# Kernel tuning notes

Measured on AMD Instinct MI355X. Metric: run time of the kernel, lower is better.

## Reference

```python
import jax, jax.numpy as jnp
from jax import lax
import numpy as np

B, N, D = 8, 8192, 64
NPOINT, RADIUS, NSAMPLE = 1024, 0.2, 32
EPS = 1e-5  # BatchNorm eps


def setup_inputs() -> dict:
    key = jax.random.key(0)
    ks = jax.random.split(key, 8)
    inp = {
        "xyz": jax.random.uniform(ks[0], (B, 3, N), dtype=jnp.float32),
        "points": jax.random.normal(ks[1], (B, D, N), dtype=jnp.float32),
    }
    dims = [(3 + D, 64), (64, 64), (64, 128)]
    for i, (ci, co) in enumerate(dims):
        inp[f"w{i}"] = jax.random.normal(ks[2 + i], (co, ci), dtype=jnp.float32) * float(1.0 / np.sqrt(ci))
        inp[f"b{i}"] = jnp.zeros((co,), jnp.float32)
        inp[f"g{i}"] = jnp.ones((co,), jnp.float32)
        inp[f"beta{i}"] = jnp.zeros((co,), jnp.float32)
    return inp


def _fps(xyz):
    # Farthest point sampling. xyz: [B, N, 3] -> idx [B, NPOINT]
    b = xyz.shape[0]

    def step(carry, _):
        dist, farthest = carry  # dist [B,N], farthest [B]
        centroid = jnp.take_along_axis(xyz, farthest[:, None, None], axis=1)  # [B,1,3]
        d = jnp.sum((xyz - centroid) ** 2, axis=-1)  # [B,N]
        dist = jnp.minimum(dist, d)
        return (dist, jnp.argmax(dist, axis=-1).astype(jnp.int32)), farthest

    init = (jnp.full((b, xyz.shape[1]), 1e10, xyz.dtype), jnp.zeros((b,), jnp.int32))
    _, idxs = lax.scan(step, init, None, length=NPOINT)  # [NPOINT, B]
    return idxs.T  # [B, NPOINT]


def _ball_query(new_xyz, xyz):
    # new_xyz: [B,S,3] centers, xyz: [B,N,3] -> neighbor idx [B,S,NSAMPLE]
    n = xyz.shape[1]
    sqr = jnp.sum((new_xyz[:, :, None, :] - xyz[:, None, :, :]) ** 2, axis=-1)  # [B,S,N]
    cand = jnp.where(sqr > RADIUS * RADIUS, n, jnp.arange(n, dtype=jnp.int32))  # N = invalid
    neg_top, _ = lax.top_k(-cand, NSAMPLE)  # smallest NSAMPLE valid indices
    idx = -neg_top  # [B,S,K], ascending; == n where fewer than K neighbors
    first = idx[..., :1]  # pad with first (closest-by-index) valid neighbor
    return jnp.where(idx == n, first, idx)


def reference(xyz, points, w0, b0, g0, beta0, w1, b1, g1, beta1, w2, b2, g2, beta2):
    xyz_t = jnp.transpose(xyz, (0, 2, 1))      # [B,N,3]
    pts_t = jnp.transpose(points, (0, 2, 1))   # [B,N,D]
    fps_idx = _fps(xyz_t)                      # [B,S]
    bidx = jnp.arange(xyz.shape[0])[:, None]
    new_xyz = xyz_t[bidx, fps_idx]             # [B,S,3]
    idx = _ball_query(new_xyz, xyz_t)          # [B,S,K]
    bidx3 = jnp.arange(xyz.shape[0])[:, None, None]
    grouped_xyz = xyz_t[bidx3, idx]            # [B,S,K,3]
    grouped_norm = grouped_xyz - new_xyz[:, :, None, :]
    grouped_pts = pts_t[bidx3, idx]            # [B,S,K,D]
    feat = jnp.concatenate([grouped_norm, grouped_pts], axis=-1)  # [B,S,K,3+D]
    # shared 1x1 Conv + BatchNorm (training-mode batch stats) + ReLU chain
    for w, b, g, bt in ((w0, b0, g0, beta0), (w1, b1, g1, beta1), (w2, b2, g2, beta2)):
        h = jnp.einsum('bskc,oc->bsko', feat, w) + b
        mean = jnp.mean(h, axis=(0, 1, 2), keepdims=True)
        var = jnp.var(h, axis=(0, 1, 2), keepdims=True)
        feat = jax.nn.relu((h - mean) * lax.rsqrt(var + EPS) * g + bt)
    pooled = jnp.max(feat, axis=2)             # max over NSAMPLE -> [B,S,C_out]
    return jnp.transpose(new_xyz, (0, 2, 1)), jnp.transpose(pooled, (0, 2, 1))
```

## Files before the change

kernel.cpp:

```cpp
#include <hip/hip_runtime.h>

#define NB 8
#define NP 8192
#define SP 1024
#define KS 32
#define CD 64
#define MROWS (NB*SP*KS)
#define NCOPY 16

typedef float v2f __attribute__((ext_vector_type(2)));
typedef unsigned long long u64;

template <int CTRL>
__device__ __forceinline__ u64 dpp_max_step(u64 x) {
    int lo = (int)(unsigned)(x & 0xffffffffull);
    int hi = (int)(unsigned)(x >> 32);
    int slo = __builtin_amdgcn_update_dpp(lo, lo, CTRL, 0xf, 0xf, false);
    int shi = __builtin_amdgcn_update_dpp(hi, hi, CTRL, 0xf, 0xf, false);
    u64 y = ((u64)(unsigned)shi << 32) | (unsigned)slo;
    return x > y ? x : y;
}

__global__ __launch_bounds__(512, 1) void k_fps_pre(const float* __restrict__ xyz,
                                                    float* __restrict__ fps_pts,
                                                    float* __restrict__ out_nx,
                                                    const float* __restrict__ points,
                                                    float* __restrict__ pts_t,
                                                    const float* __restrict__ w0,
                                                    const float* __restrict__ w1,
                                                    const float* __restrict__ w2,
                                                    float* __restrict__ Wt0,
                                                    float* __restrict__ Wt1,
                                                    float* __restrict__ Wt2,
                                                    float* __restrict__ stats)
{
#pragma clang fp contract(off)
    __shared__ __align__(16) unsigned char smem[131072 + 256];
    const int blk = blockIdx.x;
    const int t = threadIdx.x;

    if (blk >= NB) {
        if (blk >= NB + NB * (NP / 64)) {
            for (int i = t; i < 8192; i += 512) stats[i] = 0.f;
            for (int i = t; i < 64 * 67; i += 512) { int c = i / 67, kk = i % 67; Wt0[kk * 64 + c] = w0[i]; }
            for (int i = t; i < 64 * 64; i += 512) { int c = i >> 6, kk = i & 63; Wt1[kk * 64 + c] = w1[i]; }
            for (int i = t; i < 128 * 64; i += 512) { int c = i >> 6, kk = i & 63; Wt2[kk * 128 + c] = w2[i]; }
            return;
        }
        float (*tile)[65] = (float(*)[65])smem;
        const int tblk = blk - NB;
        const int b = tblk >> 7;
        const int n0 = (tblk & 127) << 6;
        const float* pb = points + (size_t)b * CD * NP;
        const int c = t & 63;
        const int dr = t >> 6;
#pragma unroll
        for (int it = 0; it < 8; ++it) {
            int d = dr + it * 8;
            tile[d][c] = pb[(size_t)d * NP + n0 + c];
        }
        __syncthreads();
#pragma unroll
        for (int it = 0; it < 8; ++it) {
            int nn = dr + it * 8;
            pts_t[((size_t)b * NP + n0 + nn) * CD + c] = tile[c][nn];
        }
        return;
    }

    float4* s_p = (float4*)smem;
    u64 (*s_wk)[8] = (u64(*)[8])(smem + 131072);
    const int b = blk;
    const int lane = t & 63, wid = t >> 6;
    const float* xb = xyz + (size_t)b * 3 * NP;
    v2f px[8], py[8], pz[8], dv[8];
#pragma unroll
    for (int j = 0; j < 8; ++j) {
        const int n0 = t + (2 * j) * 512, n1 = n0 + 512;
        px[j] = (v2f){xb[n0], xb[n1]};
        py[j] = (v2f){xb[NP + n0], xb[NP + n1]};
        pz[j] = (v2f){xb[2 * NP + n0], xb[2 * NP + n1]};
        dv[j] = (v2f){1e10f, 1e10f};
        s_p[n0] = make_float4(px[j].x, py[j].x, pz[j].x, 0.f);
        s_p[n1] = make_float4(px[j].y, py[j].y, pz[j].y, 0.f);
    }
    float cx = xb[0], cy = xb[NP], cz = xb[2 * NP];
    float hx0 = 0.f, hy0 = 0.f, hz0 = 0.f;
    float hx1 = 0.f, hy1 = 0.f, hz1 = 0.f;
    __syncthreads();
    for (int i = 0; i < SP; ++i) {
        if (i == t)       { hx0 = cx; hy0 = cy; hz0 = cz; }
        if (i == t + 512) { hx1 = cx; hy1 = cy; hz1 = cz; }
        float bv = -1.f; int bg = 0;
#pragma unroll
        for (int j = 0; j < 8; ++j) {
            v2f dx = px[j] - cx;
            v2f dy = py[j] - cy;
            v2f dz = pz[j] - cz;
            v2f d  = dx * dx + dy * dy;
            d = d + dz * dz;
            v2f dm = dv[j];
            dm.x = fminf(dm.x, d.x);
            dm.y = fminf(dm.y, d.y);
            dv[j] = dm;
            if (dm.x > bv) { bv = dm.x; bg = t + (2 * j) * 512; }
            if (dm.y > bv) { bv = dm.y; bg = t + (2 * j + 1) * 512; }
        }
        u64 bk = ((u64)__float_as_uint(bv) << 32) | (unsigned int)~bg;
        bk = dpp_max_step<0x111>(bk);
        bk = dpp_max_step<0x112>(bk);
        bk = dpp_max_step<0x114>(bk);
        bk = dpp_max_step<0x118>(bk);
        bk = dpp_max_step<0x142>(bk);
        bk = dpp_max_step<0x143>(bk);
        const int par = i & 1;
        if (lane == 63) s_wk[par][wid] = bk;
        __syncthreads();
        u64 rk = s_wk[par][lane & 7];
        rk = dpp_max_step<0x111>(rk);
        rk = dpp_max_step<0x112>(rk);
        rk = dpp_max_step<0x114>(rk);
        rk = dpp_max_step<0x118>(rk);
        const int wg = ~__builtin_amdgcn_readlane((int)(unsigned)(rk & 0xffffffffull), 15);
        const float4 c = s_p[wg];
        cx = c.x; cy = c.y; cz = c.z;
    }
    fps_pts[(b * SP + t) * 3 + 0] = hx0;
    fps_pts[(b * SP + t) * 3 + 1] = hy0;
    fps_pts[(b * SP + t) * 3 + 2] = hz0;
    fps_pts[(b * SP + t + 512) * 3 + 0] = hx1;
    fps_pts[(b * SP + t + 512) * 3 + 1] = hy1;
    fps_pts[(b * SP + t + 512) * 3 + 2] = hz1;
    out_nx[(size_t)b * 3 * SP + 0 * SP + t] = hx0;
    out_nx[(size_t)b * 3 * SP + 1 * SP + t] = hy0;
    out_nx[(size_t)b * 3 * SP + 2 * SP + t] = hz0;
    out_nx[(size_t)b * 3 * SP + 0 * SP + t + 512] = hx1;
    out_nx[(size_t)b * 3 * SP + 1 * SP + t + 512] = hy1;
    out_nx[(size_t)b * 3 * SP + 2 * SP + t + 512] = hz1;
}

__global__ __launch_bounds__(256) void k_ballquery(const float* __restrict__ xyz,
                                                   const float* __restrict__ fps_pts,
                                                   int* __restrict__ ball_idx)
{
    const int wib = threadIdx.x >> 6;
    const int lane = threadIdx.x & 63;
    const int wid = blockIdx.x * 4 + wib;
    const int b = wid >> 10;
    const float* xb = xyz + (size_t)b * 3 * NP;
    const float qx = fps_pts[wid * 3 + 0];
    const float qy = fps_pts[wid * 3 + 1];
    const float qz = fps_pts[wid * 3 + 2];
    __shared__ int s_list[4][KS];
    int* list = s_list[wib];
    const float r2 = (float)(0.2 * 0.2);
    int found = 0;
    for (int base = 0; base < NP && found < KS; base += 64) {
        int n = base + lane;
        float dx = __fsub_rn(qx, xb[n]);
        float dy = __fsub_rn(qy, xb[NP + n]);
        float dz = __fsub_rn(qz, xb[2 * NP + n]);
        float d = __fadd_rn(__fadd_rn(__fmul_rn(dx, dx), __fmul_rn(dy, dy)), __fmul_rn(dz, dz));
        bool in = !(d > r2);
        unsigned long long m = __ballot(in);
        int before = __popcll(m & ((1ull << lane) - 1ull));
        int pos = found + before;
        if (in && pos < KS) list[pos] = n;
        found += __popcll(m);
    }
    int first = list[0];
    if (lane < KS) {
        int v = (lane < found) ? list[lane] : first;
        ball_idx[wid * KS + lane] = v;
    }
}

__global__ __launch_bounds__(256) void k_layer1(const float* __restrict__ xyz,
                                                const float* __restrict__ pts_t,
                                                const float* __restrict__ fps_pts,
                                                const int* __restrict__ ball_idx,
                                                const float* __restrict__ Wt0,
                                                const float* __restrict__ bias0,
                                                float* __restrict__ h1,
                                                float* __restrict__ sum0,
                                                float* __restrict__ ssq0)
{
    __shared__ __align__(16) float Ft[67 * 128];
    __shared__ __align__(16) float Ws[67 * 64];
    __shared__ int   s_idx[128];
    __shared__ float s_q[4][3];
    const int t = threadIdx.x;
    const int m0 = blockIdx.x * 128;
    const int g0 = m0 >> 5;
    const int b = g0 >> 10;
    if (t < 128) s_idx[t] = ball_idx[g0 * KS + t];
    if (t < 12) ((float*)s_q)[t] = fps_pts[g0 * 3 + t];
    for (int i = t; i < 67 * 64; i += 256) Ws[i] = Wt0[i];
    __syncthreads();
    {
        const int r = t >> 1, half = t & 1;
        const int n = s_idx[r];
        const float* prow = pts_t + ((size_t)b * NP + n) * CD;
#pragma unroll
        for (int rep = 0; rep < 8; ++rep) {
            const int c4 = half * 4 + rep * 8;
            float4 v = *(const float4*)(prow + c4);
            Ft[(3 + c4 + 0) * 128 + r] = v.x;
            Ft[(3 + c4 + 1) * 128 + r] = v.y;
            Ft[(3 + c4 + 2) * 128 + r] = v.z;
            Ft[(3 + c4 + 3) * 128 + r] = v.w;
        }
        if (t < 128) {
            const int n2 = s_idx[t];
            const int g = t >> 5;
            const float* xb = xyz + (size_t)b * 3 * NP;
            Ft[0 * 128 + t] = __fsub_rn(xb[n2],          s_q[g][0]);
            Ft[1 * 128 + t] = __fsub_rn(xb[NP + n2],     s_q[g][1]);
            Ft[2 * 128 + t] = __fsub_rn(xb[2 * NP + n2], s_q[g][2]);
        }
    }
    __syncthreads();
    const int rg = t >> 3;
    const int cg = t & 7;
    float4 ba = *(const float4*)(bias0 + cg * 8);
    float4 bb = *(const float4*)(bias0 + cg * 8 + 4);
    float acc[4][8];
#pragma unroll
    for (int j = 0; j < 4; ++j) {
        acc[j][0] = ba.x; acc[j][1] = ba.y; acc[j][2] = ba.z; acc[j][3] = ba.w;
        acc[j][4] = bb.x; acc[j][5] = bb.y; acc[j][6] = bb.z; acc[j][7] = bb.w;
    }
    for (int kk = 0; kk < 67; ++kk) {
        float4 f = *(const float4*)(Ft + kk * 128 + rg * 4);
        float4 wa = *(const float4*)(Ws + kk * 64 + cg * 8);
        float4 wb = *(const float4*)(Ws + kk * 64 + cg * 8 + 4);
        float fv[4] = {f.x, f.y, f.z, f.w};
        float wv[8] = {wa.x, wa.y, wa.z, wa.w, wb.x, wb.y, wb.z, wb.w};
#pragma unroll
        for (int j = 0; j < 4; ++j)
#pragma unroll
            for (int i = 0; i < 8; ++i) acc[j][i] = fmaf(fv[j], wv[i], acc[j][i]);
    }
    float ls[8] = {0,0,0,0,0,0,0,0}, lq[8] = {0,0,0,0,0,0,0,0};
#pragma unroll
    for (int j = 0; j < 4; ++j) {
        int m = m0 + rg * 4 + j;
        float4 oa = {acc[j][0], acc[j][1], acc[j][2], acc[j][3]};
        float4 ob = {acc[j][4], acc[j][5], acc[j][6], acc[j][7]};
        *(float4*)(h1 + (size_t)m * 64 + cg * 8) = oa;
        *(float4*)(h1 + (size_t)m * 64 + cg * 8 + 4) = ob;
#pragma unroll
        for (int i = 0; i < 8; ++i) { float v = acc[j][i]; ls[i] += v; lq[i] += v * v; }
    }
    __syncthreads();
    float* part_s = Ft;
    float* part_q = Ft + 2048;
#pragma unroll
    for (int i = 0; i < 8; ++i) { part_s[rg * 64 + cg * 8 + i] = ls[i]; part_q[rg * 64 + cg * 8 + i] = lq[i]; }
    __syncthreads();
    if (t < 64) {
        float s = 0.f, q = 0.f;
#pragma unroll
        for (int rgi = 0; rgi < 32; ++rgi) { s += part_s[rgi * 64 + t]; q += part_q[rgi * 64 + t]; }
        int cp = blockIdx.x & (NCOPY - 1);
        atomicAdd(&sum0[cp * 64 + t], s);
        atomicAdd(&ssq0[cp * 64 + t], q);
    }
}

__global__ __launch_bounds__(256) void k_layer2(const float* __restrict__ h1,
                                                const float* __restrict__ Wt1,
                                                const float* __restrict__ bias1,
                                                const float* __restrict__ ss1,
                                                float* __restrict__ h2,
                                                float* __restrict__ sum1,
                                                float* __restrict__ ssq1)
{
    __shared__ __align__(16) float Ft[64 * 128];
    __shared__ __align__(16) float Ws[64 * 64];
    __shared__ float s_sc[64], s_sh[64];
    const int t = threadIdx.x;
    const int m0 = blockIdx.x * 128;
    for (int i = t; i < 64 * 64; i += 256) Ws[i] = Wt1[i];
    if (t < 64) { s_sc[t] = ss1[t]; s_sh[t] = ss1[64 + t]; }
    __syncthreads();
    {
        const int tq = t >> 2, qq = t & 3;
#pragma unroll
        for (int rr = 0; rr < 2; ++rr) {
            const int r = rr * 64 + tq;
            const float* hrow = h1 + (size_t)(m0 + r) * 64;
#pragma unroll
            for (int rep = 0; rep < 4; ++rep) {
                const int c4 = qq * 4 + rep * 16;
                float4 v = *(const float4*)(hrow + c4);
                Ft[(c4 + 0) * 128 + r] = fmaxf(0.f, fmaf(v.x, s_sc[c4 + 0], s_sh[c4 + 0]));
                Ft[(c4 + 1) * 128 + r] = fmaxf(0.f, fmaf(v.y, s_sc[c4 + 1], s_sh[c4 + 1]));
                Ft[(c4 + 2) * 128 + r] = fmaxf(0.f, fmaf(v.z, s_sc[c4 + 2], s_sh[c4 + 2]));
                Ft[(c4 + 3) * 128 + r] = fmaxf(0.f, fmaf(v.w, s_sc[c4 + 3], s_sh[c4 + 3]));
            }
        }
    }
    __syncthreads();
    const int rg = t >> 3;
    const int cg = t & 7;
    float4 ba = *(const float4*)(bias1 + cg * 8);
    float4 bb = *(const float4*)(bias1 + cg * 8 + 4);
    float acc[4][8];
#pragma unroll
    for (int j = 0; j < 4; ++j) {
        acc[j][0] = ba.x; acc[j][1] = ba.y; acc[j][2] = ba.z; acc[j][3] = ba.w;
        acc[j][4] = bb.x; acc[j][5] = bb.y; acc[j][6] = bb.z; acc[j][7] = bb.w;
    }
    for (int kk = 0; kk < 64; ++kk) {
        float4 f = *(const float4*)(Ft + kk * 128 + rg * 4);
        float4 wa = *(const float4*)(Ws + kk * 64 + cg * 8);
        float4 wb = *(const float4*)(Ws + kk * 64 + cg * 8 + 4);
        float fv[4] = {f.x, f.y, f.z, f.w};
        float wv[8] = {wa.x, wa.y, wa.z, wa.w, wb.x, wb.y, wb.z, wb.w};
#pragma unroll
        for (int j = 0; j < 4; ++j)
#pragma unroll
            for (int i = 0; i < 8; ++i) acc[j][i] = fmaf(fv[j], wv[i], acc[j][i]);
    }
    float ls[8] = {0,0,0,0,0,0,0,0}, lq[8] = {0,0,0,0,0,0,0,0};
#pragma unroll
    for (int j = 0; j < 4; ++j) {
        int m = m0 + rg * 4 + j;
        float4 oa = {acc[j][0], acc[j][1], acc[j][2], acc[j][3]};
        float4 ob = {acc[j][4], acc[j][5], acc[j][6], acc[j][7]};
        *(float4*)(h2 + (size_t)m * 64 + cg * 8) = oa;
        *(float4*)(h2 + (size_t)m * 64 + cg * 8 + 4) = ob;
#pragma unroll
        for (int i = 0; i < 8; ++i) { float v = acc[j][i]; ls[i] += v; lq[i] += v * v; }
    }
    __syncthreads();
    float* part_s = Ft;
    float* part_q = Ft + 2048;
#pragma unroll
    for (int i = 0; i < 8; ++i) { part_s[rg * 64 + cg * 8 + i] = ls[i]; part_q[rg * 64 + cg * 8 + i] = lq[i]; }
    __syncthreads();
    if (t < 64) {
        float s = 0.f, q = 0.f;
#pragma unroll
        for (int rgi = 0; rgi < 32; ++rgi) { s += part_s[rgi * 64 + t]; q += part_q[rgi * 64 + t]; }
        int cp = blockIdx.x & (NCOPY - 1);
        atomicAdd(&sum1[cp * 64 + t], s);
        atomicAdd(&ssq1[cp * 64 + t], q);
    }
}

__global__ __launch_bounds__(256) void k_layer3(const float* __restrict__ h2,
                                                const float* __restrict__ Wt2,
                                                const float* __restrict__ bias2,
                                                const float* __restrict__ ss2,
                                                float* __restrict__ sum2,
                                                float* __restrict__ ssq2,
                                                float* __restrict__ gmax,
                                                float* __restrict__ gmin)
{
    __shared__ __align__(16) float Ft[64 * 128];
    __shared__ __align__(16) float Ws[64 * 128];
    __shared__ float s_sc[64], s_sh[64];
    const int t = threadIdx.x;
    const int m0 = blockIdx.x * 128;
    for (int i = t; i < 64 * 128; i += 256) Ws[i] = Wt2[i];
    if (t < 64) { s_sc[t] = ss2[t]; s_sh[t] = ss2[64 + t]; }
    __syncthreads();
    {
        const int tq = t >> 2, qq = t & 3;
#pragma unroll
        for (int rr = 0; rr < 2; ++rr) {
            const int r = rr * 64 + tq;
            const float* hrow = h2 + (size_t)(m0 + r) * 64;
#pragma unroll
            for (int rep = 0; rep < 4; ++rep) {
                const int c4 = qq * 4 + rep * 16;
                float4 v = *(const float4*)(hrow + c4);
                Ft[(c4 + 0) * 128 + r] = fmaxf(0.f, fmaf(v.x, s_sc[c4 + 0], s_sh[c4 + 0]));
                Ft[(c4 + 1) * 128 + r] = fmaxf(0.f, fmaf(v.y, s_sc[c4 + 1], s_sh[c4 + 1]));
                Ft[(c4 + 2) * 128 + r] = fmaxf(0.f, fmaf(v.z, s_sc[c4 + 2], s_sh[c4 + 2]));
                Ft[(c4 + 3) * 128 + r] = fmaxf(0.f, fmaf(v.w, s_sc[c4 + 3], s_sh[c4 + 3]));
            }
        }
    }
    __syncthreads();
    const int rg = t >> 4;
    const int cg = t & 15;
    float4 ba = *(const float4*)(bias2 + cg * 8);
    float4 bb = *(const float4*)(bias2 + cg * 8 + 4);
    float acc[8][8];
#pragma unroll
    for (int j = 0; j < 8; ++j) {
        acc[j][0] = ba.x; acc[j][1] = ba.y; acc[j][2] = ba.z; acc[j][3] = ba.w;
        acc[j][4] = bb.x; acc[j][5] = bb.y; acc[j][6] = bb.z; acc[j][7] = bb.w;
    }
    for (int kk = 0; kk < 64; ++kk) {
        float4 fa = *(const float4*)(Ft + kk * 128 + rg * 8);
        float4 fb = *(const float4*)(Ft + kk * 128 + rg * 8 + 4);
        float4 wa = *(const float4*)(Ws + kk * 128 + cg * 8);
        float4 wb = *(const float4*)(Ws + kk * 128 + cg * 8 + 4);
        float fv[8] = {fa.x, fa.y, fa.z, fa.w, fb.x, fb.y, fb.z, fb.w};
        float wv[8] = {wa.x, wa.y, wa.z, wa.w, wb.x, wb.y, wb.z, wb.w};
#pragma unroll
        for (int j = 0; j < 8; ++j)
#pragma unroll
            for (int i = 0; i < 8; ++i) acc[j][i] = fmaf(fv[j], wv[i], acc[j][i]);
    }
    float ls[8] = {0,0,0,0,0,0,0,0}, lq[8] = {0,0,0,0,0,0,0,0};
    float pm[8], pn[8];
#pragma unroll
    for (int i = 0; i < 8; ++i) { pm[i] = acc[0][i]; pn[i] = acc[0][i]; }
#pragma unroll
    for (int j = 0; j < 8; ++j)
#pragma unroll
        for (int i = 0; i < 8; ++i) {
            float v = acc[j][i];
            ls[i] += v; lq[i] += v * v;
            pm[i] = fmaxf(pm[i], v); pn[i] = fminf(pn[i], v);
        }
    __syncthreads();
    float* part_s = Ft;
    float* part_q = Ft + 2048;
    float* part_m = Ft + 4096;
    float* part_n = Ft + 6144;
#pragma unroll
    for (int i = 0; i < 8; ++i) {
        part_s[rg * 128 + cg * 8 + i] = ls[i];
        part_q[rg * 128 + cg * 8 + i] = lq[i];
        part_m[rg * 128 + cg * 8 + i] = pm[i];
        part_n[rg * 128 + cg * 8 + i] = pn[i];
    }
    __syncthreads();
    if (t < 128) {
        float s = 0.f, q = 0.f;
#pragma unroll
        for (int rgi = 0; rgi < 16; ++rgi) { s += part_s[rgi * 128 + t]; q += part_q[rgi * 128 + t]; }
        int cp = blockIdx.x & (NCOPY - 1);
        atomicAdd(&sum2[cp * 128 + t], s);
        atomicAdd(&ssq2[cp * 128 + t], q);
    }
    for (int e = t; e < 512; e += 256) {
        int g = e >> 7, c = e & 127;
        float M = part_m[(g * 4 + 0) * 128 + c];
        M = fmaxf(M, part_m[(g * 4 + 1) * 128 + c]);
        M = fmaxf(M, part_m[(g * 4 + 2) * 128 + c]);
        M = fmaxf(M, part_m[(g * 4 + 3) * 128 + c]);
        float N = part_n[(g * 4 + 0) * 128 + c];
        N = fminf(N, part_n[(g * 4 + 1) * 128 + c]);
        N = fminf(N, part_n[(g * 4 + 2) * 128 + c]);
        N = fminf(N, part_n[(g * 4 + 3) * 128 + c]);
        int grp = blockIdx.x * 4 + g;
        gmax[(size_t)grp * 128 + c] = M;
        gmin[(size_t)grp * 128 + c] = N;
    }
}

__global__ __launch_bounds__(256) void k_pool2(const float* __restrict__ gmax,
                                               const float* __restrict__ gmin,
                                               const float* __restrict__ ss3,
                                               float* __restrict__ outp)
{
    int idx = blockIdx.x * 256 + threadIdx.x;
    int b = idx >> 17;
    int c = (idx >> 10) & 127;
    int s = idx & 1023;
    int grp = (b << 10) + s;
    float a = ss3[c], sh = ss3[128 + c];
    float m = (a >= 0.f) ? gmax[(size_t)grp * 128 + c] : gmin[(size_t)grp * 128 + c];
    outp[idx] = fmaxf(0.f, fmaf(m, a, sh));
}

__global__ void k_finalize(const float* __restrict__ sum, const float* __restrict__ ssq,
                           const float* __restrict__ g, const float* __restrict__ beta,
                           float* __restrict__ ss, int nc)
{
    int c = threadIdx.x;
    if (c >= nc) return;
    float s = 0.f, q = 0.f;
    for (int k = 0; k < NCOPY; ++k) { s += sum[k * nc + c]; q += ssq[k * nc + c]; }
    const float inv = 1.0f / 262144.0f;
    float mean = s * inv;
    float var = q * inv - mean * mean;
    float rstd = 1.0f / sqrtf(var + 1e-5f);
    float scale = g[c] * rstd;
    ss[c] = scale;
    ss[nc + c] = beta[c] - mean * scale;
}

extern "C" void kernel_launch(void* const* d_in, const int* in_sizes, int n_in,
                              void* d_out, int out_size, void* d_ws, size_t ws_size,
                              hipStream_t stream)
{
    const float* xyz    = (const float*)d_in[0];
    const float* points = (const float*)d_in[1];
    const float* w0 = (const float*)d_in[2];
    const float* b0 = (const float*)d_in[3];
    const float* gm0 = (const float*)d_in[4];
    const float* bt0 = (const float*)d_in[5];
    const float* w1 = (const float*)d_in[6];
    const float* b1 = (const float*)d_in[7];
    const float* gm1 = (const float*)d_in[8];
    const float* bt1 = (const float*)d_in[9];
    const float* w2 = (const float*)d_in[10];
    const float* b2 = (const float*)d_in[11];
    const float* gm2 = (const float*)d_in[12];
    const float* bt2 = (const float*)d_in[13];
    float* out = (float*)d_out;

    char* p = (char*)d_ws;
    auto alloc = [&](size_t nbytes) -> void* {
        void* r = (void*)p;
        p += (nbytes + 255) & ~(size_t)255;
        return r;
    };
    float* fps_pts = (float*)alloc((size_t)NB * SP * 3 * 4);
    int*   ball_idx = (int*)alloc((size_t)NB * SP * KS * 4);
    float* pts_t = (float*)alloc((size_t)NB * NP * CD * 4);
    float* h1 = (float*)alloc((size_t)MROWS * 64 * 4);
    float* h2 = (float*)alloc((size_t)MROWS * 64 * 4);
    float* gmax = (float*)alloc((size_t)NB * SP * 128 * 4);
    float* gmin = (float*)alloc((size_t)NB * SP * 128 * 4);
    float* Wt0 = (float*)alloc(67 * 64 * 4);
    float* Wt1 = (float*)alloc(64 * 64 * 4);
    float* Wt2 = (float*)alloc(64 * 128 * 4);
    float* stats = (float*)alloc(8192 * 4);
    float* ss1 = (float*)alloc(128 * 4);
    float* ss2 = (float*)alloc(128 * 4);
    float* ss3 = (float*)alloc(256 * 4);

    float* sum0 = stats;
    float* ssq0 = stats + 16 * 64;
    float* sum1 = stats + 2 * 16 * 64;
    float* ssq1 = stats + 3 * 16 * 64;
    float* sum2 = stats + 4 * 16 * 64;
    float* ssq2 = sum2 + 16 * 128;

    k_fps_pre<<<NB + NB * (NP / 64) + 1, 512, 0, stream>>>(
        xyz, fps_pts, out, points, pts_t, w0, w1, w2, Wt0, Wt1, Wt2, stats);
    k_ballquery<<<(NB * SP) / 4, 256, 0, stream>>>(xyz, fps_pts, ball_idx);
    k_layer1<<<MROWS / 128, 256, 0, stream>>>(xyz, pts_t, fps_pts, ball_idx, Wt0, b0, h1, sum0, ssq0);
    k_finalize<<<1, 128, 0, stream>>>(sum0, ssq0, gm0, bt0, ss1, 64);
    k_layer2<<<MROWS / 128, 256, 0, stream>>>(h1, Wt1, b1, ss1, h2, sum1, ssq1);
    k_finalize<<<1, 128, 0, stream>>>(sum1, ssq1, gm1, bt1, ss2, 64);
    k_layer3<<<MROWS / 128, 256, 0, stream>>>(h2, Wt2, b2, ss2, sum2, ssq2, gmax, gmin);
    k_finalize<<<1, 128, 0, stream>>>(sum2, ssq2, gm2, bt2, ss3, 128);
    k_pool2<<<(NB * SP * 128) / 256, 256, 0, stream>>>(gmax, gmin, ss3, out + 24576);
}
```

Baseline: 1.217 ms.

## Sort FPS points into Morton-ordered cells and skip distance updates for far waves

The FPS kernel now bins points into an 8x8x8 grid with Morton-interleaved cell ids, counting-sorts them in shared memory, and gives each thread 16 spatially contiguous points with a bounding box. Each iteration, a thread whose box lies farther from the new centroid than its current max min-distance skips the update, and whole waves skip when no lane is active. The wave's previous argmax key is then reused. This removes most of the distance arithmetic in later iterations, but adds a serial prefix scan over 512 cells, shared atomics, more registers, and a wave-level ballot branch. Ties are kept by encoding the original index into the key.

```diff
diff --git a/kernel.cpp b/kernel.cpp
--- a/kernel.cpp
+++ b/kernel.cpp
@@ -35,7 +35,7 @@
                                                     float* __restrict__ stats)
 {
 #pragma clang fp contract(off)
-    __shared__ __align__(16) unsigned char smem[131072 + 256];
+    __shared__ __align__(16) unsigned char smem[131072 + 2560];
     const int blk = blockIdx.x;
     const int t = threadIdx.x;
 
@@ -68,61 +68,106 @@
         return;
     }
 
-    float4* s_p = (float4*)smem;
-    u64 (*s_wk)[8] = (u64(*)[8])(smem + 131072);
+    float4* s_p  = (float4*)smem;
+    int*    s_cnt = (int*)(smem + 131072);
+    u64 (*s_wk)[8] = (u64(*)[8])(smem + 131072 + 2048);
     const int b = blk;
     const int lane = t & 63, wid = t >> 6;
     const float* xb = xyz + (size_t)b * 3 * NP;
-    v2f px[8], py[8], pz[8], dv[8];
-#pragma unroll
-    for (int j = 0; j < 8; ++j) {
-        const int n0 = t + (2 * j) * 512, n1 = n0 + 512;
-        px[j] = (v2f){xb[n0], xb[n1]};
-        py[j] = (v2f){xb[NP + n0], xb[NP + n1]};
-        pz[j] = (v2f){xb[2 * NP + n0], xb[2 * NP + n1]};
-        dv[j] = (v2f){1e10f, 1e10f};
-        s_p[n0] = make_float4(px[j].x, py[j].x, pz[j].x, 0.f);
-        s_p[n1] = make_float4(px[j].y, py[j].y, pz[j].y, 0.f);
+
+    float lx[16], ly[16], lz[16];
+    int   lcell[16];
+    s_cnt[t < 512 ? t : 0] = 0;
+    __syncthreads();
+#pragma unroll
+    for (int j = 0; j < 16; ++j) {
+        const int n = t + j * 512;
+        lx[j] = xb[n]; ly[j] = xb[NP + n]; lz[j] = xb[2 * NP + n];
+        int ix = (int)(lx[j] * 8.f); ix = ix < 0 ? 0 : (ix > 7 ? 7 : ix);
+        int iy = (int)(ly[j] * 8.f); iy = iy < 0 ? 0 : (iy > 7 ? 7 : iy);
+        int iz = (int)(lz[j] * 8.f); iz = iz < 0 ? 0 : (iz > 7 ? 7 : iz);
+        int sx = ((ix & 4) << 4) | ((ix & 2) << 2) | (ix & 1);
+        int sy = ((iy & 4) << 4) | ((iy & 2) << 2) | (iy & 1);
+        int sz = ((iz & 4) << 4) | ((iz & 2) << 2) | (iz & 1);
+        lcell[j] = (sx << 2) | (sy << 1) | sz;
+        atomicAdd(&s_cnt[lcell[j]], 1);
+    }
+    __syncthreads();
+    if (t == 0) {
+        int run = 0;
+        for (int c2 = 0; c2 < 512; ++c2) { int v = s_cnt[c2]; s_cnt[c2] = run; run += v; }
+    }
+    __syncthreads();
+#pragma unroll
+    for (int j = 0; j < 16; ++j) {
+        int pos = atomicAdd(&s_cnt[lcell[j]], 1);
+        s_p[pos] = make_float4(lx[j], ly[j], lz[j], __uint_as_float((unsigned)(t + j * 512)));
+    }
+    __syncthreads();
+    float px[16], py[16], pz[16], dv16[16];
+    unsigned klo[16];
+    float blx = 1e30f, bly = 1e30f, blz = 1e30f, bhx = -1e30f, bhy = -1e30f, bhz = -1e30f;
+#pragma unroll
+    for (int j = 0; j < 16; ++j) {
+        float4 v = s_p[16 * t + j];
+        px[j] = v.x; py[j] = v.y; pz[j] = v.z;
+        unsigned g = __float_as_uint(v.w);
+        klo[j] = ((8191u - g) << 13) | (unsigned)(16 * t + j);
+        dv16[j] = 1e10f;
+        blx = fminf(blx, v.x); bhx = fmaxf(bhx, v.x);
+        bly = fminf(bly, v.y); bhy = fmaxf(bhy, v.y);
+        blz = fminf(blz, v.z); bhz = fmaxf(bhz, v.z);
     }
     float cx = xb[0], cy = xb[NP], cz = xb[2 * NP];
+    float cellmax = 1e10f;
+    u64 wkey = 0;
     float hx0 = 0.f, hy0 = 0.f, hz0 = 0.f;
     float hx1 = 0.f, hy1 = 0.f, hz1 = 0.f;
     __syncthreads();
     for (int i = 0; i < SP; ++i) {
         if (i == t)       { hx0 = cx; hy0 = cy; hz0 = cz; }
         if (i == t + 512) { hx1 = cx; hy1 = cy; hz1 = cz; }
-        float bv = -1.f; int bg = 0;
-#pragma unroll
-        for (int j = 0; j < 8; ++j) {
-            v2f dx = px[j] - cx;
-            v2f dy = py[j] - cy;
-            v2f dz = pz[j] - cz;
-            v2f d  = dx * dx + dy * dy;
-            d = d + dz * dz;
-            v2f dm = dv[j];
-            dm.x = fminf(dm.x, d.x);
-            dm.y = fminf(dm.y, d.y);
-            dv[j] = dm;
-            if (dm.x > bv) { bv = dm.x; bg = t + (2 * j) * 512; }
-            if (dm.y > bv) { bv = dm.y; bg = t + (2 * j + 1) * 512; }
-        }
-        u64 bk = ((u64)__float_as_uint(bv) << 32) | (unsigned int)~bg;
-        bk = dpp_max_step<0x111>(bk);
-        bk = dpp_max_step<0x112>(bk);
-        bk = dpp_max_step<0x114>(bk);
-        bk = dpp_max_step<0x118>(bk);
-        bk = dpp_max_step<0x142>(bk);
-        bk = dpp_max_step<0x143>(bk);
+        float ddx = fmaxf(fmaxf(blx - cx, cx - bhx), 0.f);
+        float ddy = fmaxf(fmaxf(bly - cy, cy - bhy), 0.f);
+        float ddz = fmaxf(fmaxf(blz - cz, cz - bhz), 0.f);
+        float dmin = ddx * ddx + ddy * ddy;
+        dmin = dmin + ddz * ddz;
+        bool act = (dmin * 0.999f < cellmax);
+        if (__ballot(act)) {
+            u64 bk = 0; float cm = 0.f;
+#pragma unroll
+            for (int j = 0; j < 16; ++j) {
+                float dx = px[j] - cx;
+                float dy = py[j] - cy;
+                float dz = pz[j] - cz;
+                float d = dx * dx + dy * dy;
+                d = d + dz * dz;
+                float nd = fminf(dv16[j], d);
+                dv16[j] = nd;
+                cm = fmaxf(cm, nd);
+                u64 k = ((u64)__float_as_uint(nd) << 32) | klo[j];
+                bk = bk > k ? bk : k;
+            }
+            cellmax = cm;
+            bk = dpp_max_step<0x111>(bk);
+            bk = dpp_max_step<0x112>(bk);
+            bk = dpp_max_step<0x114>(bk);
+            bk = dpp_max_step<0x118>(bk);
+            bk = dpp_max_step<0x142>(bk);
+            bk = dpp_max_step<0x143>(bk);
+            wkey = bk;
+        }
         const int par = i & 1;
-        if (lane == 63) s_wk[par][wid] = bk;
+        if (lane == 63) s_wk[par][wid] = wkey;
         __syncthreads();
         u64 rk = s_wk[par][lane & 7];
         rk = dpp_max_step<0x111>(rk);
         rk = dpp_max_step<0x112>(rk);
         rk = dpp_max_step<0x114>(rk);
         rk = dpp_max_step<0x118>(rk);
-        const int wg = ~__builtin_amdgcn_readlane((int)(unsigned)(rk & 0xffffffffull), 15);
-        const float4 c = s_p[wg];
+        const int wlo = __builtin_amdgcn_readlane((int)(unsigned)(rk & 0xffffffffull), 15);
+        const int wpos = wlo & 0x1FFF;
+        const float4 c = s_p[wpos];
         cx = c.x; cy = c.y; cz = c.z;
     }
     fps_pts[(b * SP + t) * 3 + 0] = hx0;
```

After: 1.202 ms. About the same (-1.2%).
